# Kernel optimization log

Measured on AMD Instinct MI355X. Metric: run time of the kernel, lower is better.

The kernel has to match this reference:

```python
import jax, jax.numpy as jnp
import numpy as np

B, T = 8, 1024
C_IN, C_H = 4096, 4096
K_I, K_H = 3, 3
INIT_SPARSITY = 0.15


def _fixed_fanin_bipartite(rng, n_out, n_in, k):
    # exactly k True entries per row, distinct columns
    r = rng.random((n_out, n_in))
    cols = np.argsort(r, axis=1)[:, :k]
    A = np.zeros((n_out, n_in), np.float32)
    np.put_along_axis(A, cols, 1.0, axis=1)
    return A


def _fixed_fanin_graph(rng, n, k):
    # exactly k True entries per row, distinct non-self columns
    r = rng.random((n, n))
    np.fill_diagonal(r, 2.0)  # exclude self-loops
    cols = np.argsort(r, axis=1)[:, :k]
    A = np.zeros((n, n), np.float32)
    np.put_along_axis(A, cols, 1.0, axis=1)
    return A


def setup_inputs() -> dict:
    rng = np.random.default_rng(0)
    z = jnp.asarray(rng.random((B, T, C_IN)) < INIT_SPARSITY)          # bool (B,T,C_in)
    h0 = jnp.asarray(rng.random((B, C_H)) < INIT_SPARSITY)             # bool (B,C_h)
    A_input_f = jnp.asarray(_fixed_fanin_bipartite(rng, C_H, C_IN, K_I))  # (C_h,C_in) f32
    A_hidden_f = jnp.asarray(_fixed_fanin_graph(rng, C_H, K_H))           # (C_h,C_h) f32
    return {"z": z, "h0": h0, "A_input_f": A_input_f, "A_hidden_f": A_hidden_f}


def reference(z, h0, A_input_f, A_hidden_f):
    # AND-of-ORs CA: h_i(t) = [OR over input fan-in of z(t)] AND [OR over hidden fan-in of h(t-1)]
    z_tf = jnp.moveaxis(z, -2, 0)  # (T, B, C_in)

    def step(h, z_t):
        input_or = (z_t.astype(jnp.float32) @ A_input_f.T) > 0   # (B, C_h) bool
        hidden_or = (h.astype(jnp.float32) @ A_hidden_f.T) > 0   # (B, C_h) bool
        h_new = input_or & hidden_or
        return h_new, h_new

    _, h_seq = jax.lax.scan(step, h0, z_tf)   # (T, B, C_h)
    h_seq = jnp.moveaxis(h_seq, 0, -2)        # (B, T, C_h)
    return jnp.concatenate([z, h_seq], axis=-1)  # (B, T, C_in + C_h) bool
```

## Files before the change

### kernel.cpp

```cpp
#include <hip/hip_runtime.h>
#include <stdint.h>

#define B_   8
#define T_   1024
#define CIN_ 4096
#define CH_  4096


__device__ __forceinline__ uint32_t bytes_nonzero01(uint32_t w) {
  uint32_t t = (w & 0x7F7F7F7Fu) + 0x7F7F7F7Fu;
  t = (t | w) & 0x80808080u;
  return t >> 7;
}

__device__ __forceinline__ uint32_t load4(const void* base, long idx4, int es) {
  if (es == 1) {
    uint32_t w = ((const uint32_t*)base)[idx4];
    return bytes_nonzero01(w);
  } else if (es == 2) {
    uint32_t w0 = ((const uint32_t*)base)[idx4 * 2];
    uint32_t w1 = ((const uint32_t*)base)[idx4 * 2 + 1];
    uint32_t r = 0;
    r |= ((w0 & 0xFFFFu) != 0u) ? 0x00000001u : 0u;
    r |= ((w0 >> 16)     != 0u) ? 0x00000100u : 0u;
    r |= ((w1 & 0xFFFFu) != 0u) ? 0x00010000u : 0u;
    r |= ((w1 >> 16)     != 0u) ? 0x01000000u : 0u;
    return r;
  } else {
    uint4 w = ((const uint4*)base)[idx4];
    uint32_t r = 0;
    r |= (w.x != 0u) ? 0x00000001u : 0u;
    r |= (w.y != 0u) ? 0x00000100u : 0u;
    r |= (w.z != 0u) ? 0x00010000u : 0u;
    r |= (w.w != 0u) ? 0x01000000u : 0u;
    return r;
  }
}

__device__ __forceinline__ uint32_t nib4(uint32_t w) {
  return (((w & 0x01010101u) * 0x01020408u) >> 24) & 0xFu;
}

__global__ __launch_bounds__(256) void detect_kernel(const uint32_t* __restrict__ z,
                                                     uint32_t* __restrict__ modep) {
  __shared__ int sB, sH, sW, sL;
  const int n = threadIdx.x;
  if (n == 0) { sB = 1; sH = 1; sW = 1; sL = 0; }
  __syncthreads();
  int okB = 1, okH = 1, okW = 1, low = 0;
  for (int k = 0; k < 16; ++k) {
    uint32_t w = z[n + 256 * k];
    if ((w & 0xFEFEFEFEu) != 0u) okB = 0;
    uint32_t lo = w & 0xFFFFu, hi = w >> 16;
    if (!((lo == 0u || lo == 0x3F80u) && (hi == 0u || hi == 0x3F80u))) okH = 0;
    if (!(w == 0u || w == 1u)) okW = 0;
    if (lo != 0u) low = 1;
  }
  if (!okB) atomicAnd(&sB, 0);
  if (!okH) atomicAnd(&sH, 0);
  if (!okW) atomicAnd(&sW, 0);
  if (low)  atomicOr(&sL, 1);
  __syncthreads();
  if (n == 0) {
    uint32_t mode;
    if (sW)      mode = 4;
    else if (sB) mode = 1;
    else if (sH) mode = sL ? 2 : 4;
    else         mode = 1;
    modep[0] = mode;
  }
}

__global__ __launch_bounds__(256) void extract_kernel(const float* __restrict__ Ain,
                                                      const float* __restrict__ Ah,
                                                      uint32_t* __restrict__ idxin,
                                                      uint32_t* __restrict__ idxh) {
  const int wave = threadIdx.x >> 6;
  const int lane = threadIdx.x & 63;
  const int row  = blockIdx.x * 4 + wave;
  const float* A;
  uint32_t* outp;
  if (row < 4096) { A = Ain + (long)row * 4096;          outp = idxin + row * 3; }
  else            { A = Ah  + (long)(row - 4096) * 4096; outp = idxh + (row - 4096) * 3; }
  int count = 0;
  for (int it = 0; it < 64; ++it) {
    float v = A[it * 64 + lane];
    unsigned long long m = __ballot(v != 0.0f);
    if (m) {
      if (v != 0.0f) {
        int pos = count + (int)__popcll(m & ((1ull << lane) - 1ull));
        if (pos < 3) outp[pos] = (uint32_t)(it * 64 + lane);
      }
      count += (int)__popcll(m);
      if (count >= 3) break;
    }
  }
}

__global__ __launch_bounds__(1024) void inor_kernel(const void* __restrict__ z,
                                                    const uint32_t* __restrict__ idxin,
                                                    const uint32_t* __restrict__ modep,
                                                    uint32_t* __restrict__ in_orb) {
  const int t = blockIdx.x;
  const int n = threadIdx.x;
  const int es = (int)modep[0];
  __shared__ __align__(16) unsigned char zp[4096];
  uint32_t acc = 0;
  for (int b = 0; b < B_; ++b) {
    uint32_t v4 = load4(z, ((long)b * T_ + t) * 1024 + n, es);
    acc |= v4 << b;
  }
  ((uint32_t*)zp)[n] = acc;
  __syncthreads();
  const uint4* ip = (const uint4*)(idxin + n * 12);
  uint4 q0 = ip[0], q1 = ip[1], q2 = ip[2];
  uint32_t r0 = (uint32_t)zp[q0.x] | zp[q0.y] | zp[q0.z];
  uint32_t r1 = (uint32_t)zp[q0.w] | zp[q1.x] | zp[q1.y];
  uint32_t r2 = (uint32_t)zp[q1.z] | zp[q1.w] | zp[q2.x];
  uint32_t r3 = (uint32_t)zp[q2.y] | zp[q2.z] | zp[q2.w];
  in_orb[t * 1024 + n] = r0 | (r1 << 8) | (r2 << 16) | (r3 << 24);
}

__global__ __launch_bounds__(1024) void scan_kernel(const uint32_t* __restrict__ in_orb,
                                                    const uint32_t* __restrict__ idxh,
                                                    const void* __restrict__ h0,
                                                    const uint32_t* __restrict__ modep,
                                                    uint32_t* __restrict__ hbits) {
  const int b = blockIdx.x;
  const int n = threadIdx.x;
  const int es = (int)modep[0];
  __shared__ __align__(16) unsigned char hbuf[2][4096];

  uint32_t d[4][3];
  {
    const uint4* p = (const uint4*)(idxh + n * 12);
    uint4 q0 = p[0], q1 = p[1], q2 = p[2];
    d[0][0] = q0.x; d[0][1] = q0.y; d[0][2] = q0.z;
    d[1][0] = q0.w; d[1][1] = q1.x; d[1][2] = q1.y;
    d[2][0] = q1.z; d[2][1] = q1.w; d[2][2] = q2.x;
    d[3][0] = q2.y; d[3][1] = q2.z; d[3][2] = q2.w;
  }

  ((uint32_t*)hbuf[0])[n] = load4(h0, (long)b * 1024 + n, es);
  __syncthreads();

  int p = 0;
  uint32_t inw = in_orb[n];
  for (int t = 0; t < T_; ++t) {
    uint32_t inw_next = (t + 1 < T_) ? in_orb[(t + 1) * 1024 + n] : 0u;
    const unsigned char* hc = &hbuf[p][0];
    unsigned char* hn = &hbuf[p ^ 1][0];

    uint32_t mask = (inw >> b) & 0x01010101u;
    uint32_t out4 = 0;
    if (mask) {
      if (mask & 0x00000001u) {
        uint32_t v = (uint32_t)hc[d[0][0]] | hc[d[0][1]] | hc[d[0][2]];
        out4 |= v;
      }
      if (mask & 0x00000100u) {
        uint32_t v = (uint32_t)hc[d[1][0]] | hc[d[1][1]] | hc[d[1][2]];
        out4 |= v << 8;
      }
      if (mask & 0x00010000u) {
        uint32_t v = (uint32_t)hc[d[2][0]] | hc[d[2][1]] | hc[d[2][2]];
        out4 |= v << 16;
      }
      if (mask & 0x01000000u) {
        uint32_t v = (uint32_t)hc[d[3][0]] | hc[d[3][1]] | hc[d[3][2]];
        out4 |= v << 24;
      }
    }
    ((uint32_t*)hn)[n] = out4;
    __syncthreads();

    if (n < 128) {
      const uint4* hp = (const uint4*)hn;
      uint4 a = hp[n * 2];
      uint4 c = hp[n * 2 + 1];
      uint32_t wb = nib4(a.x) | (nib4(a.y) << 4) | (nib4(a.z) << 8)  | (nib4(a.w) << 12)
                  | (nib4(c.x) << 16) | (nib4(c.y) << 20) | (nib4(c.z) << 24) | (nib4(c.w) << 28);
      hbits[((long)b * T_ + t) * 128 + n] = wb;
    }
    inw = inw_next;
    p ^= 1;
  }
}

__global__ __launch_bounds__(1024) void expand_kernel(const void* __restrict__ z,
                                                      const uint32_t* __restrict__ hbits,
                                                      const uint32_t* __restrict__ modep,
                                                      uint32_t* __restrict__ out) {
  const long bt = blockIdx.x;
  const int n = threadIdx.x;
  const int es = (int)modep[0];
  __shared__ uint32_t hw[128];
  if (n < 128) hw[n] = hbits[bt * 128 + n];
  uint32_t zv = load4(z, bt * 1024 + n, es);
  __syncthreads();
  uint32_t* o = out + bt * 8192;
  uint4 zf = { zv & 1u, (zv >> 8) & 1u, (zv >> 16) & 1u, (zv >> 24) & 1u };
  ((uint4*)o)[n] = zf;
  uint32_t w = hw[n >> 3];
  uint32_t nb = (w >> ((n & 7) * 4)) & 0xFu;
  uint4 hf = { nb & 1u, (nb >> 1) & 1u, (nb >> 2) & 1u, (nb >> 3) & 1u };
  ((uint4*)(o + 4096))[n] = hf;
}

extern "C" void kernel_launch(void* const* d_in, const int* in_sizes, int n_in,
                              void* d_out, int out_size, void* d_ws, size_t ws_size,
                              hipStream_t stream) {
  const void*  z   = d_in[0];
  const void*  h0  = d_in[1];
  const float* Ain = (const float*)d_in[2];
  const float* Ah  = (const float*)d_in[3];
  uint32_t* out = (uint32_t*)d_out;

  char* ws = (char*)d_ws;
  uint32_t* modep = (uint32_t*)(ws);
  uint32_t* idxin = (uint32_t*)(ws + 256);
  uint32_t* idxh  = (uint32_t*)(ws + 256 + 49152);
  uint32_t* inorb = (uint32_t*)(ws + 98560);
  uint32_t* hbits = (uint32_t*)(ws + 98560 + 4194304);

  detect_kernel <<<1,    256,  0, stream>>>((const uint32_t*)z, modep);
  extract_kernel<<<2048, 256,  0, stream>>>(Ain, Ah, idxin, idxh);
  inor_kernel   <<<T_,   1024, 0, stream>>>(z, idxin, modep, inorb);
  scan_kernel   <<<B_,   1024, 0, stream>>>(inorb, idxh, h0, modep, hbits);
  expand_kernel <<<B_ * T_, 1024, 0, stream>>>(z, hbits, modep, out);
}
```

Measured before the change: 1.180 ms.

## Fuse output expansion into input-OR and scan kernels, drop expand kernel

Removes the separate expand kernel and the packed hbits intermediate. The z half of the output is now written by inor_kernel while it loads z, and the hidden half is written directly by scan_kernel at each timestep. This saves a kernel launch, a re-read of z and the hbits round trip. The cost is that the serial scan kernel, which runs only 8 blocks, now issues 16 KB of global stores per step, which could lengthen its critical path.

```diff
diff --git a/kernel.cpp b/kernel.cpp
--- a/kernel.cpp
+++ b/kernel.cpp
@@ -37,8 +37,9 @@
   }
 }
 
-__device__ __forceinline__ uint32_t nib4(uint32_t w) {
-  return (((w & 0x01010101u) * 0x01020408u) >> 24) & 0xFu;
+__device__ __forceinline__ uint4 expand01(uint32_t v4) {
+  uint4 r = { v4 & 1u, (v4 >> 8) & 1u, (v4 >> 16) & 1u, (v4 >> 24) & 1u };
+  return r;
 }
 
 __global__ __launch_bounds__(256) void detect_kernel(const uint32_t* __restrict__ z,
@@ -100,15 +101,18 @@
 __global__ __launch_bounds__(1024) void inor_kernel(const void* __restrict__ z,
                                                     const uint32_t* __restrict__ idxin,
                                                     const uint32_t* __restrict__ modep,
-                                                    uint32_t* __restrict__ in_orb) {
+                                                    uint32_t* __restrict__ in_orb,
+                                                    uint32_t* __restrict__ out) {
   const int t = blockIdx.x;
   const int n = threadIdx.x;
   const int es = (int)modep[0];
   __shared__ __align__(16) unsigned char zp[4096];
   uint32_t acc = 0;
+  #pragma unroll
   for (int b = 0; b < B_; ++b) {
     uint32_t v4 = load4(z, ((long)b * T_ + t) * 1024 + n, es);
     acc |= v4 << b;
+    ((uint4*)(out + ((long)b * T_ + t) * 8192))[n] = expand01(v4);
   }
   ((uint32_t*)zp)[n] = acc;
   __syncthreads();
@@ -125,7 +129,7 @@
                                                     const uint32_t* __restrict__ idxh,
                                                     const void* __restrict__ h0,
                                                     const uint32_t* __restrict__ modep,
-                                                    uint32_t* __restrict__ hbits) {
+                                                    uint32_t* __restrict__ out) {
   const int b = blockIdx.x;
   const int n = threadIdx.x;
   const int es = (int)modep[0];
@@ -144,6 +148,8 @@
   ((uint32_t*)hbuf[0])[n] = load4(h0, (long)b * 1024 + n, es);
   __syncthreads();
 
+  uint32_t* outh = out + (long)b * T_ * 8192 + 4096;
+
   int p = 0;
   uint32_t inw = in_orb[n];
   for (int t = 0; t < T_; ++t) {
@@ -172,39 +178,12 @@
       }
     }
     ((uint32_t*)hn)[n] = out4;
+    ((uint4*)(outh + (long)t * 8192))[n] = expand01(out4);
     __syncthreads();
 
-    if (n < 128) {
-      const uint4* hp = (const uint4*)hn;
-      uint4 a = hp[n * 2];
-      uint4 c = hp[n * 2 + 1];
-      uint32_t wb = nib4(a.x) | (nib4(a.y) << 4) | (nib4(a.z) << 8)  | (nib4(a.w) << 12)
-                  | (nib4(c.x) << 16) | (nib4(c.y) << 20) | (nib4(c.z) << 24) | (nib4(c.w) << 28);
-      hbits[((long)b * T_ + t) * 128 + n] = wb;
-    }
     inw = inw_next;
     p ^= 1;
   }
-}
-
-__global__ __launch_bounds__(1024) void expand_kernel(const void* __restrict__ z,
-                                                      const uint32_t* __restrict__ hbits,
-                                                      const uint32_t* __restrict__ modep,
-                                                      uint32_t* __restrict__ out) {
-  const long bt = blockIdx.x;
-  const int n = threadIdx.x;
-  const int es = (int)modep[0];
-  __shared__ uint32_t hw[128];
-  if (n < 128) hw[n] = hbits[bt * 128 + n];
-  uint32_t zv = load4(z, bt * 1024 + n, es);
-  __syncthreads();
-  uint32_t* o = out + bt * 8192;
-  uint4 zf = { zv & 1u, (zv >> 8) & 1u, (zv >> 16) & 1u, (zv >> 24) & 1u };
-  ((uint4*)o)[n] = zf;
-  uint32_t w = hw[n >> 3];
-  uint32_t nb = (w >> ((n & 7) * 4)) & 0xFu;
-  uint4 hf = { nb & 1u, (nb >> 1) & 1u, (nb >> 2) & 1u, (nb >> 3) & 1u };
-  ((uint4*)(o + 4096))[n] = hf;
 }
 
 extern "C" void kernel_launch(void* const* d_in, const int* in_sizes, int n_in,
@@ -221,11 +200,9 @@
   uint32_t* idxin = (uint32_t*)(ws + 256);
   uint32_t* idxh  = (uint32_t*)(ws + 256 + 49152);
   uint32_t* inorb = (uint32_t*)(ws + 98560);
-  uint32_t* hbits = (uint32_t*)(ws + 98560 + 4194304);
 
   detect_kernel <<<1,    256,  0, stream>>>((const uint32_t*)z, modep);
   extract_kernel<<<2048, 256,  0, stream>>>(Ain, Ah, idxin, idxh);
-  inor_kernel   <<<T_,   1024, 0, stream>>>(z, idxin, modep, inorb);
-  scan_kernel   <<<B_,   1024, 0, stream>>>(inorb, idxh, h0, modep, hbits);
-  expand_kernel <<<B_ * T_, 1024, 0, stream>>>(z, hbits, modep, out);
-}
+  inor_kernel   <<<T_,   1024, 0, stream>>>(z, idxin, modep, inorb, out);
+  scan_kernel   <<<B_,   1024, 0, stream>>>(inorb, idxh, h0, modep, out);
+}
```

New measurement: 960.4 us. -18.6%, faster.
